# Kernel tuning notes

Measured on AMD Instinct MI355X. Metric: run time of the kernel, lower is better.

## Reference

```python
import jax, jax.numpy as jnp
import numpy as np

B, N, P, K = 64, 64, 128, 16

def setup_inputs() -> dict:
    key = jax.random.key(0)
    k1, k2, k3, k4 = jax.random.split(key, 4)
    x = jax.random.normal(k1, (B, N, P), dtype=jnp.float32)
    idx = jax.random.randint(k2, (B, P), 0, K)
    x_mask = jax.nn.one_hot(idx, K, dtype=jnp.float32)  # [B, P, K] one-hot
    # xavier_normal_ init for weights [K, N*N]
    std = float(np.sqrt(2.0 / (K + N * N)))
    weights = std * jax.random.normal(k3, (K, N * N), dtype=jnp.float32)
    g = jax.random.uniform(k4, (N * N, N * N), dtype=jnp.float32)
    return {"x": x, "x_mask": x_mask, "weights": weights, "g": g}

def reference(x, x_mask, weights, g):
    b, n, p = x.shape
    wg = jnp.matmul(weights ** 2, g)               # [K, N*N]
    w = jnp.einsum('bpk,km->bpm', x_mask, wg)      # [B, P, N*N]
    ef = jnp.exp(-w.reshape(b, p, n, n))           # [B, P, N, N]
    # torch does x[b].reshape(p, -1, 1): row-major reinterpretation of [N,P] -> [P,N]
    xr = x.reshape(b, p, n)                        # [B, P, N]
    Z = jnp.einsum('bpij,bpj->bi', ef, xr)         # batched matvec, summed over p
    return (Z, w)
```

## Files before the change

kernel.cpp:

```cpp
#include <hip/hip_runtime.h>
#include <hip/hip_bf16.h>


__device__ __forceinline__ void dma16(const void* g, void* l) {
    __builtin_amdgcn_global_load_lds(
        (const __attribute__((address_space(1))) void*)g,
        (__attribute__((address_space(3))) void*)l, 16, 0, 0);
}

__global__ __launch_bounds__(256) void k_gemm(const float* __restrict__ W,
                                              const float* __restrict__ G,
                                              float* __restrict__ part) {
    __shared__ float buf[8192];
    float4* w2t4 = (float4*)buf;
    float4* stg  = (float4*)(buf + 4096);

    const int tc  = blockIdx.x & 15;
    const int mg  = blockIdx.x >> 4;
    const int tid = threadIdx.x;
    const int wv  = tid >> 6;
    const int ln  = tid & 63;
    const int tt  = tid >> 4;
    const int t0  = tc * 256;

    {
        float v[16];
#pragma unroll
        for (int k = 0; k < 16; ++k) {
            float w = W[k * 4096 + t0 + tid];
            v[k] = w * w;
        }
#pragma unroll
        for (int q = 0; q < 4; ++q)
            w2t4[tid * 4 + q] = make_float4(v[4*q], v[4*q+1], v[4*q+2], v[4*q+3]);
    }

    const float4* G4 = (const float4*)G;
    const int fi  = wv * 64 + ln;
    const int tl_ = fi >> 4;
    const int mc_ = fi & 15;

    dma16(&G4[(size_t)(t0 + tl_) * 1024 + mg * 16 + mc_], &stg[wv * 64]);
    __syncthreads();

    float4 acc[16];
#pragma unroll
    for (int k = 0; k < 16; ++k) acc[k] = make_float4(0.f, 0.f, 0.f, 0.f);

    for (int s = 0; s < 16; ++s) {
        if (s < 15)
            dma16(&G4[(size_t)(t0 + (s + 1) * 16 + tl_) * 1024 + mg * 16 + mc_],
                  &stg[((s + 1) & 1) * 256 + wv * 64]);

        const float4 g4 = stg[(s & 1) * 256 + tid];
        const float4* wr = &w2t4[(s * 16 + tt) * 4];
#pragma unroll
        for (int q = 0; q < 4; ++q) {
            const float4 wq = wr[q];
            const float* wf = (const float*)&wq;
#pragma unroll
            for (int c = 0; c < 4; ++c) {
                const float sc = wf[c];
                acc[q*4+c].x = fmaf(sc, g4.x, acc[q*4+c].x);
                acc[q*4+c].y = fmaf(sc, g4.y, acc[q*4+c].y);
                acc[q*4+c].z = fmaf(sc, g4.z, acc[q*4+c].z);
                acc[q*4+c].w = fmaf(sc, g4.w, acc[q*4+c].w);
            }
        }
        __syncthreads();
    }

    float4* red = (float4*)buf;
    float4* p4  = (float4*)part;
    const int col = tid & 15;
    (void)col;
#pragma unroll
    for (int r = 0; r < 2; ++r) {
#pragma unroll
        for (int ks = 0; ks < 8; ++ks)
            red[ks * 256 + tid] = acc[r * 8 + ks];
        __syncthreads();
        if (tid < 128) {
            const int ks = tid >> 4;
            const int c2 = tid & 15;
            float4 s = make_float4(0.f, 0.f, 0.f, 0.f);
#pragma unroll
            for (int t2 = 0; t2 < 16; ++t2) {
                float4 v = red[ks * 256 + t2 * 16 + c2];
                s.x += v.x; s.y += v.y; s.z += v.z; s.w += v.w;
            }
            const int k = r * 8 + ks;
            p4[(size_t)tc * 16384 + (size_t)k * 1024 + mg * 16 + c2] = s;
        }
        __syncthreads();
    }
}

__global__ __launch_bounds__(256) void k_reduce(const float* __restrict__ part,
                                                float* __restrict__ wg,
                                                float* __restrict__ E) {
    const int q = blockIdx.x * 256 + threadIdx.x;
    const float4* p4 = (const float4*)part;
    float4 s = make_float4(0.f, 0.f, 0.f, 0.f);
#pragma unroll
    for (int tc = 0; tc < 16; ++tc) {
        float4 v = p4[(size_t)tc * 16384 + q];
        s.x += v.x; s.y += v.y; s.z += v.z; s.w += v.w;
    }
    ((float4*)wg)[q] = s;
    ((float4*)E)[q] = make_float4(expf(-s.x), expf(-s.y), expf(-s.z), expf(-s.w));
}

__global__ __launch_bounds__(256) void k_wz(const float* __restrict__ x,
                                            const float* __restrict__ xmask,
                                            const float* __restrict__ wg,
                                            const float* __restrict__ E,
                                            float* __restrict__ wout,
                                            float* __restrict__ zout) {
    __shared__ float sw[4][16][64];
    __shared__ int   idx[128];
    __shared__ float zr[16][16];
    const int tid = threadIdx.x;

    if (blockIdx.x < 8192) {
        const int bp = blockIdx.x;
        const float* xm = xmask + (size_t)bp * 16;
        int k = 0;
#pragma unroll
        for (int i = 0; i < 16; ++i) k = (xm[i] > 0.5f) ? i : k;
        const float4* src = (const float4*)(wg + (size_t)k * 4096);
        float4*       dst = (float4*)(wout + (size_t)bp * 4096);
#pragma unroll
        for (int c = 0; c < 4; ++c)
            dst[c * 256 + tid] = src[c * 256 + tid];
        return;
    }

    const int zb = blockIdx.x - 8192;
    const int b  = zb >> 2;
    const int iq = zb & 3;
    const int wv = tid >> 6;
    const int ln = tid & 63;

    if (tid < 128) {
        const float* xm = xmask + ((size_t)b * 128 + tid) * 16;
        int k = 0;
#pragma unroll
        for (int i = 0; i < 16; ++i) k = (xm[i] > 0.5f) ? i : k;
        idx[tid] = k;
    }
#pragma unroll
    for (int c = 0; c < 16; ++c)
        ((float*)sw)[c * 256 + tid] = 0.f;
    __syncthreads();

    const float* xb = x + (size_t)b * 8192;
    for (int p = wv * 32; p < wv * 32 + 32; ++p) {
        int k = idx[p];
        sw[wv][k][ln] += xb[p * 64 + ln];
    }
    __syncthreads();

    for (int e = tid; e < 1024; e += 256) {
        int k2 = e >> 6, j = e & 63;
        sw[0][k2][j] = sw[0][k2][j] + sw[1][k2][j] + sw[2][k2][j] + sw[3][k2][j];
    }
    __syncthreads();

    {
        const int k  = tid >> 4;
        const int il = tid & 15;
        const int i  = iq * 16 + il;
        float a = 0.f;
        const float4* Er = (const float4*)(E + (size_t)k * 4096 + i * 64);
        const float4* sr = (const float4*)(&sw[0][k][0]);
#pragma unroll
        for (int j4 = 0; j4 < 16; ++j4) {
            float4 e4 = Er[j4];
            float4 s4 = sr[j4];
            a = fmaf(e4.x, s4.x, a);
            a = fmaf(e4.y, s4.y, a);
            a = fmaf(e4.z, s4.z, a);
            a = fmaf(e4.w, s4.w, a);
        }
        zr[k][il] = a;
    }
    __syncthreads();
    if (tid < 16) {
        float s = 0.f;
#pragma unroll
        for (int k = 0; k < 16; ++k) s += zr[k][tid];
        zout[b * 64 + iq * 16 + tid] = s;
    }
}

extern "C" void kernel_launch(void* const* d_in, const int* in_sizes, int n_in,
                              void* d_out, int out_size, void* d_ws, size_t ws_size,
                              hipStream_t stream) {
    const float* x     = (const float*)d_in[0];
    const float* xmask = (const float*)d_in[1];
    const float* W     = (const float*)d_in[2];
    const float* G     = (const float*)d_in[3];

    float* zout = (float*)d_out;
    float* wout = (float*)d_out + 4096;

    float* wg = (float*)d_ws;
    float* E  = wg + 65536;

    float* part = wout;

    k_gemm  <<<1024, 256, 0, stream>>>(W, G, part);
    k_reduce<<<64,   256, 0, stream>>>(part, wg, E);
    k_wz    <<<8448, 256, 0, stream>>>(x, xmask, wg, E, wout, zout);
}
```

Before: 50.62 us.

## Move x-bucketing into GEMM launch, double K-step per iteration, copy two rows per block

The per-batch scatter-add of x into 16 mask buckets moves out of the final kernel and into 64 extra blocks of the GEMM launch, which write the bucket sums to workspace. This takes that work off the critical path of the last kernel and overlaps it with the GEMM. The GEMM loop now processes two 16-row G tiles per iteration with two DMAs, which halves the barrier count. The broadcast-copy blocks of the final kernel each handle two output rows, halving the block count. In exchange the Z blocks read bucket sums from global memory, and the extra workspace buffer adds memory traffic.

```diff
diff --git a/kernel.cpp b/kernel.cpp
--- a/kernel.cpp
+++ b/kernel.cpp
@@ -10,16 +10,43 @@
 
 __global__ __launch_bounds__(256) void k_gemm(const float* __restrict__ W,
                                               const float* __restrict__ G,
-                                              float* __restrict__ part) {
+                                              float* __restrict__ part,
+                                              const float* __restrict__ x,
+                                              const float* __restrict__ xmask,
+                                              float* __restrict__ sbuf) {
     __shared__ float buf[8192];
-    float4* w2t4 = (float4*)buf;
-    float4* stg  = (float4*)(buf + 4096);
-
-    const int tc  = blockIdx.x & 15;
-    const int mg  = blockIdx.x >> 4;
     const int tid = threadIdx.x;
     const int wv  = tid >> 6;
     const int ln  = tid & 63;
+
+    if (blockIdx.x >= 1024) {
+        const int b = blockIdx.x - 1024;
+        float* sw  = buf;
+        int*  idxp = (int*)(buf + 4096);
+        if (tid < 128) {
+            const float* xm = xmask + ((size_t)b * 128 + tid) * 16;
+            int k = 0;
+#pragma unroll
+            for (int i = 0; i < 16; ++i) k = (xm[i] > 0.5f) ? i : k;
+            idxp[tid] = k;
+        }
+#pragma unroll
+        for (int c = 0; c < 16; ++c) sw[c * 256 + tid] = 0.f;
+        __syncthreads();
+        const float* xb = x + (size_t)b * 8192;
+        for (int p = wv * 32; p < wv * 32 + 32; ++p)
+            sw[wv * 1024 + idxp[p] * 64 + ln] += xb[p * 64 + ln];
+        __syncthreads();
+        for (int e = tid; e < 1024; e += 256)
+            sbuf[b * 1024 + e] = sw[e] + sw[1024 + e] + sw[2048 + e] + sw[3072 + e];
+        return;
+    }
+
+    float4* w2t4 = (float4*)buf;
+    float4* stg  = (float4*)(buf + 4096);
+
+    const int tc  = blockIdx.x & 15;
+    const int mg  = blockIdx.x >> 4;
     const int tt  = tid >> 4;
     const int t0  = tc * 256;
 
@@ -36,35 +63,44 @@
     }
 
     const float4* G4 = (const float4*)G;
-    const int fi  = wv * 64 + ln;
-    const int tl_ = fi >> 4;
-    const int mc_ = fi & 15;
-
-    dma16(&G4[(size_t)(t0 + tl_) * 1024 + mg * 16 + mc_], &stg[wv * 64]);
+    const int tl_ = tid >> 4;
+    const int mc_ = tid & 15;
+    const size_t gbase = (size_t)mg * 16 + mc_;
+
+    dma16(&G4[(size_t)(t0 + tl_) * 1024 + gbase],      &stg[wv * 64]);
+    dma16(&G4[(size_t)(t0 + 16 + tl_) * 1024 + gbase], &stg[256 + wv * 64]);
     __syncthreads();
 
     float4 acc[16];
 #pragma unroll
     for (int k = 0; k < 16; ++k) acc[k] = make_float4(0.f, 0.f, 0.f, 0.f);
 
-    for (int s = 0; s < 16; ++s) {
-        if (s < 15)
-            dma16(&G4[(size_t)(t0 + (s + 1) * 16 + tl_) * 1024 + mg * 16 + mc_],
-                  &stg[((s + 1) & 1) * 256 + wv * 64]);
-
-        const float4 g4 = stg[(s & 1) * 256 + tid];
-        const float4* wr = &w2t4[(s * 16 + tt) * 4];
+    for (int s = 0; s < 8; ++s) {
+        if (s < 7) {
+            const int tn = t0 + (s + 1) * 32;
+            const int db = ((s + 1) & 1) * 512;
+            dma16(&G4[(size_t)(tn + tl_) * 1024 + gbase],      &stg[db + wv * 64]);
+            dma16(&G4[(size_t)(tn + 16 + tl_) * 1024 + gbase], &stg[db + 256 + wv * 64]);
+        }
+        const int db = (s & 1) * 512;
+        const float4 g4a = stg[db + tid];
+        const float4 g4b = stg[db + 256 + tid];
+        const float4* wra = &w2t4[(s * 32 + tt) * 4];
+        const float4* wrb = &w2t4[(s * 32 + 16 + tt) * 4];
 #pragma unroll
         for (int q = 0; q < 4; ++q) {
-            const float4 wq = wr[q];
-            const float* wf = (const float*)&wq;
+            const float4 wqa = wra[q];
+            const float4 wqb = wrb[q];
+            const float* wfa = (const float*)&wqa;
+            const float* wfb = (const float*)&wqb;
 #pragma unroll
             for (int c = 0; c < 4; ++c) {
-                const float sc = wf[c];
-                acc[q*4+c].x = fmaf(sc, g4.x, acc[q*4+c].x);
-                acc[q*4+c].y = fmaf(sc, g4.y, acc[q*4+c].y);
-                acc[q*4+c].z = fmaf(sc, g4.z, acc[q*4+c].z);
-                acc[q*4+c].w = fmaf(sc, g4.w, acc[q*4+c].w);
+                const float sa = wfa[c];
+                const float sb = wfb[c];
+                acc[q*4+c].x = fmaf(sa, g4a.x, fmaf(sb, g4b.x, acc[q*4+c].x));
+                acc[q*4+c].y = fmaf(sa, g4a.y, fmaf(sb, g4b.y, acc[q*4+c].y));
+                acc[q*4+c].z = fmaf(sa, g4a.z, fmaf(sb, g4b.z, acc[q*4+c].z));
+                acc[q*4+c].w = fmaf(sa, g4a.w, fmaf(sb, g4b.w, acc[q*4+c].w));
             }
         }
         __syncthreads();
@@ -72,8 +108,6 @@
 
     float4* red = (float4*)buf;
     float4* p4  = (float4*)part;
-    const int col = tid & 15;
-    (void)col;
 #pragma unroll
     for (int r = 0; r < 2; ++r) {
 #pragma unroll
@@ -111,69 +145,25 @@
     ((float4*)E)[q] = make_float4(expf(-s.x), expf(-s.y), expf(-s.z), expf(-s.w));
 }
 
-__global__ __launch_bounds__(256) void k_wz(const float* __restrict__ x,
-                                            const float* __restrict__ xmask,
+__global__ __launch_bounds__(256) void k_wz(const float* __restrict__ xmask,
                                             const float* __restrict__ wg,
                                             const float* __restrict__ E,
+                                            const float* __restrict__ sbuf,
                                             float* __restrict__ wout,
                                             float* __restrict__ zout) {
-    __shared__ float sw[4][16][64];
-    __shared__ int   idx[128];
     __shared__ float zr[16][16];
     const int tid = threadIdx.x;
 
-    if (blockIdx.x < 8192) {
-        const int bp = blockIdx.x;
-        const float* xm = xmask + (size_t)bp * 16;
-        int k = 0;
-#pragma unroll
-        for (int i = 0; i < 16; ++i) k = (xm[i] > 0.5f) ? i : k;
-        const float4* src = (const float4*)(wg + (size_t)k * 4096);
-        float4*       dst = (float4*)(wout + (size_t)bp * 4096);
-#pragma unroll
-        for (int c = 0; c < 4; ++c)
-            dst[c * 256 + tid] = src[c * 256 + tid];
-        return;
-    }
-
-    const int zb = blockIdx.x - 8192;
-    const int b  = zb >> 2;
-    const int iq = zb & 3;
-    const int wv = tid >> 6;
-    const int ln = tid & 63;
-
-    if (tid < 128) {
-        const float* xm = xmask + ((size_t)b * 128 + tid) * 16;
-        int k = 0;
-#pragma unroll
-        for (int i = 0; i < 16; ++i) k = (xm[i] > 0.5f) ? i : k;
-        idx[tid] = k;
-    }
-#pragma unroll
-    for (int c = 0; c < 16; ++c)
-        ((float*)sw)[c * 256 + tid] = 0.f;
-    __syncthreads();
-
-    const float* xb = x + (size_t)b * 8192;
-    for (int p = wv * 32; p < wv * 32 + 32; ++p) {
-        int k = idx[p];
-        sw[wv][k][ln] += xb[p * 64 + ln];
-    }
-    __syncthreads();
-
-    for (int e = tid; e < 1024; e += 256) {
-        int k2 = e >> 6, j = e & 63;
-        sw[0][k2][j] = sw[0][k2][j] + sw[1][k2][j] + sw[2][k2][j] + sw[3][k2][j];
-    }
-    __syncthreads();
-
-    {
+    if (blockIdx.x < 256) {
+        const int zb = blockIdx.x;
+        const int b  = zb >> 2;
+        const int iq = zb & 3;
         const int k  = tid >> 4;
         const int il = tid & 15;
         const int i  = iq * 16 + il;
         float a = 0.f;
         const float4* Er = (const float4*)(E + (size_t)k * 4096 + i * 64);
-        const float4* sr = (const float4*)(&sw[0][k][0]);
+        const float4* sr = (const float4*)(sbuf + (size_t)b * 1024 + k * 64);
 #pragma unroll
         for (int j4 = 0; j4 < 16; ++j4) {
             float4 e4 = Er[j4];
@@ -184,14 +174,35 @@
             a = fmaf(e4.w, s4.w, a);
         }
         zr[k][il] = a;
-    }
-    __syncthreads();
-    if (tid < 16) {
-        float s = 0.f;
-#pragma unroll
-        for (int k = 0; k < 16; ++k) s += zr[k][tid];
-        zout[b * 64 + iq * 16 + tid] = s;
-    }
+        __syncthreads();
+        if (tid < 16) {
+            float s = 0.f;
+#pragma unroll
+            for (int kk = 0; kk < 16; ++kk) s += zr[kk][tid];
+            zout[b * 64 + iq * 16 + tid] = s;
+        }
+        return;
+    }
+
+    const int wb = blockIdx.x - 256;
+    const float* xm0 = xmask + (size_t)(wb * 2) * 16;
+    const float* xm1 = xm0 + 16;
+    int k0 = 0, k1 = 0;
+#pragma unroll
+    for (int i = 0; i < 16; ++i) {
+        k0 = (xm0[i] > 0.5f) ? i : k0;
+        k1 = (xm1[i] > 0.5f) ? i : k1;
+    }
+    const float4* s0 = (const float4*)(wg + (size_t)k0 * 4096);
+    const float4* s1 = (const float4*)(wg + (size_t)k1 * 4096);
+    float4* d0 = (float4*)(wout + (size_t)(wb * 2) * 4096);
+    float4* d1 = d0 + 1024;
+#pragma unroll
+    for (int c = 0; c < 4; ++c)
+        d0[c * 256 + tid] = s0[c * 256 + tid];
+#pragma unroll
+    for (int c = 0; c < 4; ++c)
+        d1[c * 256 + tid] = s1[c * 256 + tid];
 }
 
 extern "C" void kernel_launch(void* const* d_in, const int* in_sizes, int n_in,
@@ -205,12 +216,13 @@
     float* zout = (float*)d_out;
     float* wout = (float*)d_out + 4096;
 
-    float* wg = (float*)d_ws;
-    float* E  = wg + 65536;
+    float* wg   = (float*)d_ws;
+    float* E    = wg + 65536;
+    float* sbuf = E + 65536;
 
     float* part = wout;
 
-    k_gemm  <<<1024, 256, 0, stream>>>(W, G, part);
+    k_gemm  <<<1088, 256, 0, stream>>>(W, G, part, x, xmask, sbuf);
     k_reduce<<<64,   256, 0, stream>>>(part, wg, E);
-    k_wz    <<<8448, 256, 0, stream>>>(x, xmask, wg, E, wout, zout);
-}
+    k_wz    <<<4352, 256, 0, stream>>>(xmask, wg, E, sbuf, wout, zout);
+}
```

After: 55.29 us. 1.09x slower.
